# Optimization experiments

Measured on AMD Instinct MI355X. Metric: run time of the kernel, lower is better.

## Reference

```python
import jax, jax.numpy as jnp
import numpy as np

D_MODEL = 768
N_HEADS = 12
D_K = D_MODEL // N_HEADS
BATCH = 1
SEQ = 4096


def setup_inputs() -> dict:
    key = jax.random.key(0)
    kx, kq, kk, kv, ko = jax.random.split(key, 5)
    s = 1.0 / np.sqrt(D_MODEL)
    return {
        "x": jax.random.normal(kx, (BATCH, SEQ, D_MODEL), dtype=jnp.float32),
        "wq": jax.random.normal(kq, (D_MODEL, D_MODEL), dtype=jnp.float32) * s,
        "wk": jax.random.normal(kk, (D_MODEL, D_MODEL), dtype=jnp.float32) * s,
        "wv": jax.random.normal(kv, (D_MODEL, D_MODEL), dtype=jnp.float32) * s,
        "wo": jax.random.normal(ko, (D_MODEL, D_MODEL), dtype=jnp.float32) * s,
    }


def reference(x, wq, wk, wv, wo):
    B, S, D = x.shape
    H, dk = N_HEADS, D_K
    # nn.Linear(x) = x @ W.T ; reshape to [B,H,S,dk]
    def proj(w):
        return (x @ w.T).reshape(B, S, H, dk).transpose(0, 2, 1, 3)
    q, k, v = proj(wq), proj(wk), proj(wv)
    scores = jnp.einsum('bhqd,bhkd->bhqk', q, k) / np.sqrt(dk).astype(np.float32)
    attn = jax.nn.softmax(scores, axis=-1)
    out = jnp.einsum('bhqk,bhkd->bhqd', attn, v)
    out = out.transpose(0, 2, 1, 3).reshape(B, S, D)
    return out @ wo.T
```

## Files before the change

### kernel.cpp

```cpp
#include <hip/hip_runtime.h>
#include <stdint.h>

#define SEQ 4096
#define DMODEL 768
#define NHEADS 12
#define DKH 64

typedef __attribute__((ext_vector_type(8))) short short8;
typedef __attribute__((ext_vector_type(4))) float floatx4;

__device__ __forceinline__ unsigned short f2bf(float f) {
    unsigned int u = __float_as_uint(f);
    u += 0x7fffu + ((u >> 16) & 1u);
    return (unsigned short)(u >> 16);
}

__device__ __forceinline__ float exp2fast(float x) {
    return __builtin_amdgcn_exp2f(x);
}

__device__ __forceinline__ unsigned int cvt_pk_bf16(float lo, float hi) {
    unsigned int r;
    asm("v_cvt_pk_bf16_f32 %0, %1, %2" : "=v"(r) : "v"(lo), "v"(hi));
    return r;
}

__device__ __forceinline__ int swz(int row, int colb) {
    return colb ^ ((row & 7) << 4);
}

__device__ __forceinline__ void async_copy16(void* lds, const void* g) {
    __builtin_amdgcn_global_load_lds(
        (const __attribute__((address_space(1))) void*)g,
        (__attribute__((address_space(3))) void*)lds,
        16, 0, 0);
}

__global__ __launch_bounds__(256) void castk(const float* __restrict__ src,
                                             unsigned short* __restrict__ dst,
                                             int n4) {
    int i = blockIdx.x * 256 + threadIdx.x;
    if (i >= n4) return;
    float4 v = ((const float4*)src)[i];
    ushort4 o;
    o.x = f2bf(v.x); o.y = f2bf(v.y); o.z = f2bf(v.z); o.w = f2bf(v.w);
    ((ushort4*)dst)[i] = o;
}

__global__ __launch_bounds__(256) void castw(const float* __restrict__ w0,
                                             const float* __restrict__ w1,
                                             const float* __restrict__ w2,
                                             const float* __restrict__ w3,
                                             unsigned short* __restrict__ dst) {
    int b = blockIdx.x;
    int wsel = b / 576;
    int i = (b % 576) * 256 + threadIdx.x;
    const float* src = (wsel == 0) ? w0 : (wsel == 1) ? w1 : (wsel == 2) ? w2 : w3;
    float4 v = ((const float4*)src)[i];
    ushort4 o;
    o.x = f2bf(v.x); o.y = f2bf(v.y); o.z = f2bf(v.z); o.w = f2bf(v.w);
    ((ushort4*)(dst + (size_t)wsel * 589824))[i] = o;
}

#define STAGE_G(bsel, kb)                                                              \
    do {                                                                               \
        char* As_ = smem + (bsel) * 24576;                                             \
        _Pragma("unroll") for (int ii = 0; ii < 4; ii++) {                             \
            int o = ii * 4096 + t * 16;                                                \
            int row = o >> 7, colb = o & 127;                                          \
            async_copy16(As_ + ii * 4096 + wid * 1024,                                 \
                         (const char*)A + ((size_t)(rowBase + row) * DMODEL + (kb)) * 2 \
                             + swz(row, colb));                                        \
        }                                                                              \
        _Pragma("unroll") for (int ii = 0; ii < 2; ii++) {                             \
            int o = ii * 4096 + t * 16;                                                \
            int row = o >> 7, colb = o & 127;                                          \
            async_copy16(As_ + 16384 + ii * 4096 + wid * 1024,                         \
                         (const char*)B + ((size_t)(colBase + row) * DMODEL + (kb)) * 2 \
                             + swz(row, colb));                                        \
        }                                                                              \
    } while (0)

#define GEMM_COMPUTE(As, Bs)                                                           \
    do {                                                                               \
        short8 a_[4][2], b_[2][2];                                                     \
        _Pragma("unroll") for (int m = 0; m < 4; m++)                                  \
            _Pragma("unroll") for (int kk = 0; kk < 2; kk++) {                         \
                int row = wr * 64 + m * 16 + lr;                                       \
                int colb = kk * 64 + lg * 16;                                          \
                a_[m][kk] = *(const short8*)((As) + row * 128 + swz(row, colb));       \
            }                                                                          \
        _Pragma("unroll") for (int n = 0; n < 2; n++)                                  \
            _Pragma("unroll") for (int kk = 0; kk < 2; kk++) {                         \
                int row = wc * 32 + n * 16 + lr;                                       \
                int colb = kk * 64 + lg * 16;                                          \
                b_[n][kk] = *(const short8*)((Bs) + row * 128 + swz(row, colb));       \
            }                                                                          \
        _Pragma("unroll") for (int m = 0; m < 4; m++)                                  \
            _Pragma("unroll") for (int n = 0; n < 2; n++)                              \
                _Pragma("unroll") for (int kk = 0; kk < 2; kk++)                       \
                    acc[m][n] = __builtin_amdgcn_mfma_f32_16x16x32_bf16(               \
                        a_[m][kk], b_[n][kk], acc[m][n], 0, 0, 0);                     \
    } while (0)

__global__ __launch_bounds__(256, 2)
void gemm_qkv(const unsigned short* __restrict__ A,
              const unsigned short* __restrict__ W,
              unsigned short* __restrict__ OutBase, float qscale) {
    __shared__ __align__(128) char smem[49152];

    const int t = threadIdx.x;
    const int wid = t >> 6, lane = t & 63;
    const int lr = lane & 15, lg = lane >> 4;
    const int wr = wid >> 1, wc = wid & 1;
    const int rowBase = blockIdx.x * 128;
    const int proj = blockIdx.y / 12;
    const int colBase = (blockIdx.y % 12) * 64;
    const unsigned short* B = W + (size_t)proj * 589824;

    const floatx4 zero4 = {0.f, 0.f, 0.f, 0.f};
    floatx4 acc[4][2];
#pragma unroll
    for (int m = 0; m < 4; m++)
#pragma unroll
        for (int n = 0; n < 2; n++) acc[m][n] = zero4;

    STAGE_G(0, 0);
    for (int i = 0; i < 12; ++i) {
        __builtin_amdgcn_s_barrier();
        __builtin_amdgcn_sched_barrier(0);
        if (i < 11) {
            STAGE_G((i + 1) & 1, (i + 1) * 64);
            asm volatile("s_waitcnt vmcnt(6)" ::: "memory");
        } else {
            asm volatile("s_waitcnt vmcnt(0)" ::: "memory");
        }
        __builtin_amdgcn_s_barrier();
        __builtin_amdgcn_sched_barrier(0);
        char* As = smem + (i & 1) * 24576;
        GEMM_COMPUTE(As, As + 16384);
    }

    if (proj < 2) {
        unsigned short* O = OutBase + (size_t)proj * 3145728;
        float scale = (proj == 0) ? qscale : 1.0f;
#pragma unroll
        for (int m = 0; m < 4; m++)
#pragma unroll
            for (int n = 0; n < 2; n++)
#pragma unroll
                for (int r = 0; r < 4; r++) {
                    int srow = rowBase + wr * 64 + m * 16 + lg * 4 + r;
                    int col = colBase + wc * 32 + n * 16 + lr;
                    int h = col >> 6, d = col & 63;
                    O[((size_t)h * SEQ + srow) * DKH + d] = f2bf(acc[m][n][r] * scale);
                }
    } else {
        unsigned short* O = OutBase + 6291456;
#pragma unroll
        for (int m = 0; m < 4; m++)
#pragma unroll
            for (int n = 0; n < 2; n++) {
                int srow0 = rowBase + wr * 64 + m * 16 + lg * 4;
                int z = srow0 & 31;
                int pos0 = (srow0 & ~31) + 8 * ((z >> 2) & 3) + 4 * (z >> 4);
                int col = colBase + wc * 32 + n * 16 + lr;
                ushort4 o4;
                o4.x = f2bf(acc[m][n][0]);
                o4.y = f2bf(acc[m][n][1]);
                o4.z = f2bf(acc[m][n][2]);
                o4.w = f2bf(acc[m][n][3]);
                *(ushort4*)(O + (size_t)col * SEQ + pos0) = o4;
            }
    }
}

__global__ __launch_bounds__(256, 2)
void gemm_o(const unsigned short* __restrict__ A,
            const unsigned short* __restrict__ B,
            float* __restrict__ Out) {
    __shared__ __align__(128) char smem[49152];

    const int t = threadIdx.x;
    const int wid = t >> 6, lane = t & 63;
    const int lr = lane & 15, lg = lane >> 4;
    const int wr = wid >> 1, wc = wid & 1;
    const int rowBase = blockIdx.x * 128;
    const int colBase = blockIdx.y * 64;

    const floatx4 zero4 = {0.f, 0.f, 0.f, 0.f};
    floatx4 acc[4][2];
#pragma unroll
    for (int m = 0; m < 4; m++)
#pragma unroll
        for (int n = 0; n < 2; n++) acc[m][n] = zero4;

    STAGE_G(0, 0);
    for (int i = 0; i < 12; ++i) {
        __builtin_amdgcn_s_barrier();
        __builtin_amdgcn_sched_barrier(0);
        if (i < 11) {
            STAGE_G((i + 1) & 1, (i + 1) * 64);
            asm volatile("s_waitcnt vmcnt(6)" ::: "memory");
        } else {
            asm volatile("s_waitcnt vmcnt(0)" ::: "memory");
        }
        __builtin_amdgcn_s_barrier();
        __builtin_amdgcn_sched_barrier(0);
        char* As = smem + (i & 1) * 24576;
        GEMM_COMPUTE(As, As + 16384);
    }

#pragma unroll
    for (int m = 0; m < 4; m++)
#pragma unroll
        for (int n = 0; n < 2; n++)
#pragma unroll
            for (int r = 0; r < 4; r++) {
                int srow = rowBase + wr * 64 + m * 16 + lg * 4 + r;
                int col = colBase + wc * 32 + n * 16 + lr;
                Out[(size_t)srow * DMODEL + col] = acc[m][n][r];
            }
}

#define STAGE_A(bsel, kv0)                                                             \
    do {                                                                               \
        char* Kd_ = smem + (bsel) * 16384;                                             \
        _Pragma("unroll") for (int ii = 0; ii < 2; ii++) {                             \
            int o = ii * 4096 + t * 16;                                                \
            int row = o >> 7, colb = o & 127;                                          \
            async_copy16(Kd_ + ii * 4096 + wid * 1024,                                 \
                         (const char*)(Kp + headOff + (size_t)((kv0) + row) * DKH)     \
                             + swz(row, colb));                                        \
        }                                                                              \
        _Pragma("unroll") for (int ii = 0; ii < 2; ii++) {                             \
            int o = ii * 4096 + t * 16;                                                \
            int row = o >> 7, colb = o & 127;                                          \
            async_copy16(Kd_ + 8192 + ii * 4096 + wid * 1024,                          \
                         (const char*)(Vt + (size_t)(h * DKH + row) * SEQ + (kv0))     \
                             + swz(row, colb));                                        \
        }                                                                              \
    } while (0)

__global__ __launch_bounds__(256, 4)
void attn_k(const unsigned short* __restrict__ Q,
            const unsigned short* __restrict__ Kp,
            const unsigned short* __restrict__ Vt,
            unsigned short* __restrict__ AO) {
    __shared__ __align__(128) char smem[49152];

    const int t = threadIdx.x;
    const int wid = t >> 6, lane = t & 63;
    const int lr = lane & 15, lg = lane >> 4;

    int nid = (blockIdx.x & 7) * 96 + (blockIdx.x >> 3);
    const int h = nid >> 6, qb = nid & 63;
    const size_t headOff = (size_t)h * SEQ * DKH;

    const unsigned short* qptr = Q + headOff + (size_t)(qb * 64 + wid * 16 + lr) * DKH + lg * 8;
    short8 qf[2];
    qf[0] = *(const short8*)qptr;
    qf[1] = *(const short8*)(qptr + 32);

    const short8 ones8 = {(short)0x3F80, (short)0x3F80, (short)0x3F80, (short)0x3F80,
                          (short)0x3F80, (short)0x3F80, (short)0x3F80, (short)0x3F80};
    const floatx4 zero4 = {0.f, 0.f, 0.f, 0.f};
    float mrun = -3.0e38f;
    floatx4 acc[4];
    floatx4 acc_l = zero4;
#pragma unroll
    for (int f = 0; f < 4; f++) acc[f] = zero4;

    STAGE_A(0, 0);
    STAGE_A(1, 64);

    int cA = 0;
    for (int tt = 0; tt < 64; ++tt) {
        if (tt < 62) asm volatile("s_waitcnt vmcnt(4)" ::: "memory");
        else         asm volatile("s_waitcnt vmcnt(0)" ::: "memory");
        __builtin_amdgcn_s_barrier();
        __builtin_amdgcn_sched_barrier(0);
        if (tt < 62) {
            int cC = cA + 2; if (cC >= 3) cC -= 3;
            STAGE_A(cC, (tt + 2) * 64);
        }
        char* Ks = smem + cA * 16384;
        char* Vs = Ks + 8192;

        floatx4 s[4];
#pragma unroll
        for (int ct = 0; ct < 4; ct++) s[ct] = zero4;
#pragma unroll
        for (int ct = 0; ct < 4; ct++)
#pragma unroll
            for (int kk = 0; kk < 2; kk++) {
                int row = ct * 16 + lr;
                int colb = kk * 64 + lg * 16;
                short8 kf = *(const short8*)(Ks + row * 128 + swz(row, colb));
                s[ct] = __builtin_amdgcn_mfma_f32_16x16x32_bf16(kf, qf[kk], s[ct], 0, 0, 0);
            }

        float mt = s[0][0];
#pragma unroll
        for (int ct = 0; ct < 4; ct++)
            mt = fmaxf(fmaxf(fmaxf(mt, s[ct][0]), fmaxf(s[ct][1], s[ct][2])), s[ct][3]);
        mt = fmaxf(mt, __shfl_xor(mt, 16));
        mt = fmaxf(mt, __shfl_xor(mt, 32));
        if (!__all(mt <= mrun + 8.0f)) {
            float mnew = fmaxf(mrun, mt);
            float al = exp2fast(mrun - mnew);
#pragma unroll
            for (int f = 0; f < 4; f++)
#pragma unroll
                for (int r = 0; r < 4; r++) acc[f][r] *= al;
            acc_l[0] *= al;
            mrun = mnew;
        }
#pragma unroll
        for (int ct = 0; ct < 4; ct++)
#pragma unroll
            for (int r = 0; r < 4; r++) s[ct][r] = exp2fast(s[ct][r] - mrun);

#pragma unroll
        for (int kk = 0; kk < 2; kk++) {
            uint4 pw;
            pw.x = cvt_pk_bf16(s[2 * kk][0], s[2 * kk][1]);
            pw.y = cvt_pk_bf16(s[2 * kk][2], s[2 * kk][3]);
            pw.z = cvt_pk_bf16(s[2 * kk + 1][0], s[2 * kk + 1][1]);
            pw.w = cvt_pk_bf16(s[2 * kk + 1][2], s[2 * kk + 1][3]);
            short8 pf = *(const short8*)&pw;
#pragma unroll
            for (int f = 0; f < 4; f++) {
                int row = f * 16 + lr;
                int byteo = (row * 128 + kk * 64 + lg * 16) ^ ((row & 7) << 4);
                short8 vf = *(const short8*)(Vs + byteo);
                acc[f] = __builtin_amdgcn_mfma_f32_16x16x32_bf16(vf, pf, acc[f], 0, 0, 0);
            }
            acc_l = __builtin_amdgcn_mfma_f32_16x16x32_bf16(ones8, pf, acc_l, 0, 0, 0);
        }

        cA = (cA == 2) ? 0 : cA + 1;
    }

    float inv = 1.0f / acc_l[0];
    int srow = qb * 64 + wid * 16 + lr;
#pragma unroll
    for (int f = 0; f < 4; f++) {
        ushort4 o4;
        o4.x = f2bf(acc[f][0] * inv);
        o4.y = f2bf(acc[f][1] * inv);
        o4.z = f2bf(acc[f][2] * inv);
        o4.w = f2bf(acc[f][3] * inv);
        int col = h * DKH + f * 16 + lg * 4;
        *(ushort4*)(AO + (size_t)srow * DMODEL + col) = o4;
    }
}

extern "C" void kernel_launch(void* const* d_in, const int* in_sizes, int n_in,
                              void* d_out, int out_size, void* d_ws, size_t ws_size,
                              hipStream_t stream) {
    const float* x  = (const float*)d_in[0];
    const float* wq = (const float*)d_in[1];
    const float* wk = (const float*)d_in[2];
    const float* wv = (const float*)d_in[3];
    const float* wo = (const float*)d_in[4];

    char* ws = (char*)d_ws;
    unsigned short* xb  = (unsigned short*)(ws + 0);
    unsigned short* wqb = (unsigned short*)(ws + 6291456);
    unsigned short* wob = (unsigned short*)(ws + 9830400);
    unsigned short* Qb  = (unsigned short*)(ws + 11010048);
    unsigned short* Kb  = (unsigned short*)(ws + 17301504);
    unsigned short* VTb = (unsigned short*)(ws + 23592960);
    unsigned short* AOb = (unsigned short*)(ws + 29884416);

    castk<<<3072, 256, 0, stream>>>(x, xb, 786432);
    castw<<<2304, 256, 0, stream>>>(wq, wk, wv, wo, wqb);

    gemm_qkv<<<dim3(32, 36), 256, 0, stream>>>(xb, wqb, Qb, 0.18033688f);

    attn_k<<<dim3(768), 256, 0, stream>>>(Qb, Kb, VTb, AOb);

    gemm_o<<<dim3(32, 12), 256, 0, stream>>>(AOb, wob, (float*)d_out);
}
```

Baseline: 132.8 us.

## Restructure attention loop to 128-key tiles with split K/V staging

The attention kernel now processes 128 keys per iteration instead of 64, halving loop trips and barriers. K tiles are double-buffered and loaded one iteration ahead, while the V tile for the current step is loaded into a single buffer during the QK^T and softmax phase, with a second barrier before the PV MFMAs. MFMA sections are wrapped in s_setprio, and occupancy hint drops from 4 to 3 blocks per CU. This adds register pressure (8 score tiles) and exposes V load latency within the iteration rather than prefetching it a full step ahead.

```diff
diff --git a/kernel.cpp b/kernel.cpp
--- a/kernel.cpp
+++ b/kernel.cpp
@@ -223,26 +223,31 @@
             }
 }
 
-#define STAGE_A(bsel, kv0)                                                             \
+#define STAGE_KA(bsel, kv0)                                                            \
     do {                                                                               \
         char* Kd_ = smem + (bsel) * 16384;                                             \
-        _Pragma("unroll") for (int ii = 0; ii < 2; ii++) {                             \
+        _Pragma("unroll") for (int ii = 0; ii < 4; ii++) {                             \
             int o = ii * 4096 + t * 16;                                                \
             int row = o >> 7, colb = o & 127;                                          \
             async_copy16(Kd_ + ii * 4096 + wid * 1024,                                 \
                          (const char*)(Kp + headOff + (size_t)((kv0) + row) * DKH)     \
                              + swz(row, colb));                                        \
         }                                                                              \
-        _Pragma("unroll") for (int ii = 0; ii < 2; ii++) {                             \
+    } while (0)
+
+#define STAGE_VA(kv0)                                                                  \
+    do {                                                                               \
+        char* Vd_ = smem + 32768;                                                      \
+        _Pragma("unroll") for (int ii = 0; ii < 4; ii++) {                             \
             int o = ii * 4096 + t * 16;                                                \
-            int row = o >> 7, colb = o & 127;                                          \
-            async_copy16(Kd_ + 8192 + ii * 4096 + wid * 1024,                          \
+            int row = o >> 8, colb = o & 255;                                          \
+            async_copy16(Vd_ + ii * 4096 + wid * 1024,                                 \
                          (const char*)(Vt + (size_t)(h * DKH + row) * SEQ + (kv0))     \
                              + swz(row, colb));                                        \
         }                                                                              \
     } while (0)
 
-__global__ __launch_bounds__(256, 4)
+__global__ __launch_bounds__(256, 3)
 void attn_k(const unsigned short* __restrict__ Q,
             const unsigned short* __restrict__ Kp,
             const unsigned short* __restrict__ Vt,
@@ -271,27 +276,25 @@
 #pragma unroll
     for (int f = 0; f < 4; f++) acc[f] = zero4;
 
-    STAGE_A(0, 0);
-    STAGE_A(1, 64);
-
-    int cA = 0;
-    for (int tt = 0; tt < 64; ++tt) {
-        if (tt < 62) asm volatile("s_waitcnt vmcnt(4)" ::: "memory");
-        else         asm volatile("s_waitcnt vmcnt(0)" ::: "memory");
-        __builtin_amdgcn_s_barrier();
-        __builtin_amdgcn_sched_barrier(0);
-        if (tt < 62) {
-            int cC = cA + 2; if (cC >= 3) cC -= 3;
-            STAGE_A(cC, (tt + 2) * 64);
-        }
-        char* Ks = smem + cA * 16384;
-        char* Vs = Ks + 8192;
-
-        floatx4 s[4];
-#pragma unroll
-        for (int ct = 0; ct < 4; ct++) s[ct] = zero4;
-#pragma unroll
-        for (int ct = 0; ct < 4; ct++)
+    STAGE_KA(0, 0);
+
+    for (int tt = 0; tt < 32; ++tt) {
+        asm volatile("s_waitcnt vmcnt(0)" ::: "memory");
+        __builtin_amdgcn_s_barrier();
+        __builtin_amdgcn_sched_barrier(0);
+        STAGE_VA(tt * 128);
+        if (tt < 31) STAGE_KA((tt + 1) & 1, (tt + 1) * 128);
+        __builtin_amdgcn_sched_barrier(0);
+
+        char* Ks = smem + (tt & 1) * 16384;
+        char* Vs = smem + 32768;
+
+        floatx4 s[8];
+#pragma unroll
+        for (int ct = 0; ct < 8; ct++) s[ct] = zero4;
+        __builtin_amdgcn_s_setprio(1);
+#pragma unroll
+        for (int ct = 0; ct < 8; ct++)
 #pragma unroll
             for (int kk = 0; kk < 2; kk++) {
                 int row = ct * 16 + lr;
@@ -299,11 +302,14 @@
                 short8 kf = *(const short8*)(Ks + row * 128 + swz(row, colb));
                 s[ct] = __builtin_amdgcn_mfma_f32_16x16x32_bf16(kf, qf[kk], s[ct], 0, 0, 0);
             }
-
-        float mt = s[0][0];
-#pragma unroll
-        for (int ct = 0; ct < 4; ct++)
-            mt = fmaxf(fmaxf(fmaxf(mt, s[ct][0]), fmaxf(s[ct][1], s[ct][2])), s[ct][3]);
+        __builtin_amdgcn_s_setprio(0);
+
+        float cm[8];
+#pragma unroll
+        for (int ct = 0; ct < 8; ct++)
+            cm[ct] = fmaxf(fmaxf(s[ct][0], s[ct][1]), fmaxf(s[ct][2], s[ct][3]));
+        float mt = fmaxf(fmaxf(fmaxf(cm[0], cm[1]), fmaxf(cm[2], cm[3])),
+                         fmaxf(fmaxf(cm[4], cm[5]), fmaxf(cm[6], cm[7])));
         mt = fmaxf(mt, __shfl_xor(mt, 16));
         mt = fmaxf(mt, __shfl_xor(mt, 32));
         if (!__all(mt <= mrun + 8.0f)) {
@@ -317,12 +323,18 @@
             mrun = mnew;
         }
 #pragma unroll
-        for (int ct = 0; ct < 4; ct++)
+        for (int ct = 0; ct < 8; ct++)
 #pragma unroll
             for (int r = 0; r < 4; r++) s[ct][r] = exp2fast(s[ct][r] - mrun);
 
-#pragma unroll
-        for (int kk = 0; kk < 2; kk++) {
+        if (tt < 31) asm volatile("s_waitcnt vmcnt(4)" ::: "memory");
+        else         asm volatile("s_waitcnt vmcnt(0)" ::: "memory");
+        __builtin_amdgcn_s_barrier();
+        __builtin_amdgcn_sched_barrier(0);
+
+        __builtin_amdgcn_s_setprio(1);
+#pragma unroll
+        for (int kk = 0; kk < 4; kk++) {
             uint4 pw;
             pw.x = cvt_pk_bf16(s[2 * kk][0], s[2 * kk][1]);
             pw.y = cvt_pk_bf16(s[2 * kk][2], s[2 * kk][3]);
@@ -332,14 +344,13 @@
 #pragma unroll
             for (int f = 0; f < 4; f++) {
                 int row = f * 16 + lr;
-                int byteo = (row * 128 + kk * 64 + lg * 16) ^ ((row & 7) << 4);
+                int byteo = (row * 256 + kk * 64 + lg * 16) ^ ((row & 7) << 4);
                 short8 vf = *(const short8*)(Vs + byteo);
                 acc[f] = __builtin_amdgcn_mfma_f32_16x16x32_bf16(vf, pf, acc[f], 0, 0, 0);
             }
             acc_l = __builtin_amdgcn_mfma_f32_16x16x32_bf16(ones8, pf, acc_l, 0, 0, 0);
         }
-
-        cA = (cA == 2) ? 0 : cA + 1;
+        __builtin_amdgcn_s_setprio(0);
     }
 
     float inv = 1.0f / acc_l[0];
```

New measurement: 118.5 us. 10.8% less time.
